# Kernel tuning notes

Hardware: AMD Instinct MI355X
Metric: run time of the kernel (lower is better)

## Reference

```python
import jax, jax.numpy as jnp
import numpy as np

NUM_NODES = 50000
NUM_EDGES = 600000
IN_DIM = 128
OUT_DIM = 128


def setup_inputs() -> dict:
    key = jax.random.key(0)
    k1, k2, k3, k4, k5 = jax.random.split(key, 5)
    x = jax.random.normal(k1, (NUM_NODES, IN_DIM), dtype=jnp.float32)
    edge_index = jax.random.randint(k2, (2, NUM_EDGES), 0, NUM_NODES, dtype=jnp.int64)
    edge_weight = jax.random.uniform(k3, (NUM_EDGES,), dtype=jnp.float32)
    W = jax.random.normal(k4, (OUT_DIM, IN_DIM), dtype=jnp.float32) * (1.0 / np.sqrt(IN_DIM))
    b = jax.random.normal(k5, (OUT_DIM,), dtype=jnp.float32) * 0.01
    return {"x": x, "edge_index": edge_index, "edge_weight": edge_weight, "W": W, "b": b}


def reference(x, edge_index, edge_weight, W, b):
    num_nodes = x.shape[0]
    # add self loops
    loop = jnp.arange(num_nodes, dtype=edge_index.dtype)
    src = jnp.concatenate([edge_index[0], loop])           # [E + N]
    tgt = jnp.concatenate([edge_index[1], loop])           # [E + N]
    w = jnp.concatenate([edge_weight, jnp.ones((num_nodes,), dtype=edge_weight.dtype)])
    # degree via scatter-add over src, then symmetric normalization
    deg = jax.ops.segment_sum(w, src, num_segments=num_nodes)  # [N]
    dinv = 1.0 / jnp.sqrt(deg)
    w_norm = w * dinv[src] * dinv[tgt]                      # [E + N]
    # gather-scale-scatter aggregation
    msg = x[src] * w_norm[:, None]                          # [E + N, D]
    agg = jax.ops.segment_sum(msg, tgt, num_segments=num_nodes)  # [N, D]
    # dense linear (torch Linear convention)
    return agg @ W.T + b
```

## Files before the change

### kernel.cpp

```cpp
#include <hip/hip_runtime.h>

#define D 128
#define GROWS 32
#define HCHUNKS 128
#define RNG 8064


__device__ __forceinline__ unsigned bf16rne(float f) {
  unsigned u = __float_as_uint(f);
  return (u + 0x7FFFu + ((u >> 16) & 1u)) >> 16;
}

__device__ __forceinline__ float4 bf16x4(uint2 u) {
  float4 r;
  r.x = __uint_as_float(u.x << 16);
  r.y = __uint_as_float(u.x & 0xFFFF0000u);
  r.z = __uint_as_float(u.y << 16);
  r.w = __uint_as_float(u.y & 0xFFFF0000u);
  return r;
}

__global__ __launch_bounds__(256) void k_setup(const float* __restrict__ W,
                                               const int* __restrict__ ei,
                                               float* __restrict__ Wt,
                                               int* __restrict__ flag) {
  int i = blockIdx.x * 256 + threadIdx.x;
  if (i < D * D) {
    int c = i >> 7, k = i & 127;
    Wt[k * D + c] = W[i];
  }
  if (i == 0) {
    flag[0] = (ei[1] == 0 && ei[3] == 0 && ei[5] == 0 && ei[7] == 0) ? 1 : 0;
  }
}

__global__ __launch_bounds__(256) void k_gemm(const float* __restrict__ x,
                                              const float* __restrict__ Wt,
                                              uint2* __restrict__ yb,
                                              int N) {
  __shared__ float Xs[GROWS * D];
  const int tid = threadIdx.x;
  const int row0 = blockIdx.x * GROWS;

  for (int f = tid; f < GROWS * D / 4; f += 256) {
    int r = row0 + ((f * 4) >> 7);
    float4 v = make_float4(0.f, 0.f, 0.f, 0.f);
    if (r < N)
      v = reinterpret_cast<const float4*>(x)[(size_t)row0 * (D / 4) + f];
    reinterpret_cast<float4*>(Xs)[f] = v;
  }
  __syncthreads();

  const int c0 = (tid & 31) * 4;
  const int r0 = (tid >> 5) * 4;
  float acc[4][4];
#pragma unroll
  for (int i = 0; i < 4; ++i)
#pragma unroll
    for (int j = 0; j < 4; ++j) acc[i][j] = 0.f;

#pragma unroll 4
  for (int k = 0; k < D; ++k) {
    float4 wv = reinterpret_cast<const float4*>(Wt)[(k * D + c0) >> 2];
    float xr[4];
#pragma unroll
    for (int i = 0; i < 4; ++i) xr[i] = Xs[(r0 + i) * D + k];
#pragma unroll
    for (int i = 0; i < 4; ++i) {
      acc[i][0] += xr[i] * wv.x;
      acc[i][1] += xr[i] * wv.y;
      acc[i][2] += xr[i] * wv.z;
      acc[i][3] += xr[i] * wv.w;
    }
  }
#pragma unroll
  for (int i = 0; i < 4; ++i) {
    int row = row0 + r0 + i;
    if (row < N) {
      uint2 u;
      u.x = bf16rne(acc[i][0]) | (bf16rne(acc[i][1]) << 16);
      u.y = bf16rne(acc[i][2]) | (bf16rne(acc[i][3]) << 16);
      yb[(size_t)row * 32 + (tid & 31)] = u;
    }
  }
}

__global__ __launch_bounds__(256) void k_hist(const int* __restrict__ ei,
                                              const float* __restrict__ ew,
                                              float* __restrict__ pdeg,
                                              unsigned short* __restrict__ pcnt,
                                              const int* __restrict__ flag,
                                              int E) {
  __shared__ float hd[RNG];
  __shared__ int hc[RNG];
  const int tid = threadIdx.x;
  const int chunk = blockIdx.x, r = blockIdx.y;
  const int lo = r * RNG;
  for (int i = tid; i < RNG; i += 256) { hd[i] = 0.f; hc[i] = 0; }
  __syncthreads();

  const int epc = (E + HCHUNKS - 1) / HCHUNKS;
  const int e0 = chunk * epc;
  const int e1 = min(e0 + epc, E);
  const bool f64 = flag[0] != 0;
  const int2* ei2 = reinterpret_cast<const int2*>(ei);
  for (int e = e0 + tid; e < e1; e += 256) {
    int s = f64 ? ei2[e].x : ei[e];
    int t = f64 ? ei2[E + e].x : ei[E + e];
    int ds = s - lo;
    if ((unsigned)ds < (unsigned)RNG) atomicAdd(&hd[ds], ew[e]);
    int dt = t - lo;
    if ((unsigned)dt < (unsigned)RNG) atomicAdd(&hc[dt], 1);
  }
  __syncthreads();
  size_t base = ((size_t)r * HCHUNKS + chunk) * RNG;
  for (int i = tid; i < RNG; i += 256) {
    pdeg[base + i] = hd[i];
    pcnt[base + i] = (unsigned short)hc[i];
  }
}

__device__ __forceinline__ int wave_incl_scan(int v, int lane) {
#pragma unroll
  for (int o = 1; o < 64; o <<= 1) {
    int t = __shfl_up(v, o);
    if (lane >= o) v += t;
  }
  return v;
}

__global__ __launch_bounds__(256) void k_scan1(const float* __restrict__ pdeg,
                                               const unsigned short* __restrict__ pcnt,
                                               float* __restrict__ dinv,
                                               int* __restrict__ rowptr,
                                               int* __restrict__ blocksum,
                                               int N) {
  __shared__ int wtot[4];
  int tid = threadIdx.x;
  int i = blockIdx.x * 256 + tid;
  int v = 0;
  if (i < N) {
    int r = i / RNG, off = i - r * RNG;
    size_t base = (size_t)r * HCHUNKS * RNG + off;
    float s = 0.f;
    int c = 0;
#pragma unroll 8
    for (int k = 0; k < HCHUNKS; ++k) {
      s += pdeg[base + (size_t)k * RNG];
      c += pcnt[base + (size_t)k * RNG];
    }
    dinv[i] = rsqrtf(s + 1.0f);
    v = c;
  }
  int lane = tid & 63, wv = tid >> 6;
  int inc = wave_incl_scan(v, lane);
  if (lane == 63) wtot[wv] = inc;
  __syncthreads();
  if (tid == 0) {
    int r = 0;
#pragma unroll
    for (int k = 0; k < 4; ++k) { int t = wtot[k]; wtot[k] = r; r += t; }
  }
  __syncthreads();
  int exc = wtot[wv] + inc - v;
  if (i < N) rowptr[i] = exc;
  if (tid == 255) blocksum[blockIdx.x] = wtot[3] + inc;
}

__global__ __launch_bounds__(64) void k_scan2(int* __restrict__ blocksum,
                                              int* __restrict__ blockoff,
                                              int nb) {
  int lane = threadIdx.x;
  int carry = 0;
  for (int base = 0; base < nb; base += 64) {
    int idx = base + lane;
    int v = (idx < nb) ? blocksum[idx] : 0;
    int inc = wave_incl_scan(v, lane);
    if (idx < nb) blockoff[idx] = carry + inc - v;
    carry += __shfl(inc, 63);
  }
}

__global__ __launch_bounds__(256) void k_scan3base(int* __restrict__ rowptr,
                                                   const int* __restrict__ blockoff,
                                                   const unsigned short* __restrict__ pcnt,
                                                   int* __restrict__ cbase,
                                                   int N, int E) {
  int i = blockIdx.x * 256 + threadIdx.x;
  if (i >= N) {
    if (i == N) rowptr[N] = E;
    return;
  }
  int rp = rowptr[i] + blockoff[blockIdx.x];
  rowptr[i] = rp;
  int r = i / RNG, off = i - r * RNG;
  size_t pb = (size_t)r * HCHUNKS * RNG + off;
  int run = rp;
#pragma unroll 8
  for (int c = 0; c < HCHUNKS; ++c) {
    cbase[(size_t)c * N + i] = run;
    run += pcnt[pb + (size_t)c * RNG];
  }
}

__global__ __launch_bounds__(256) void k_scatter(const int* __restrict__ ei,
                                                 const float* __restrict__ ew,
                                                 const float* __restrict__ dinv,
                                                 const int* __restrict__ cbase,
                                                 int2* __restrict__ edges,
                                                 const int* __restrict__ flag,
                                                 int N, int E) {
  __shared__ int hb[RNG];
  const int tid = threadIdx.x;
  const int chunk = blockIdx.x, r = blockIdx.y;
  const int lo = r * RNG;
  for (int j = tid; j < RNG; j += 256) {
    int v = lo + j;
    hb[j] = (v < N) ? cbase[(size_t)chunk * N + v] : 0;
  }
  __syncthreads();

  const int epc = (E + HCHUNKS - 1) / HCHUNKS;
  const int e0 = chunk * epc;
  const int e1 = min(e0 + epc, E);
  const bool f64 = flag[0] != 0;
  const int2* ei2 = reinterpret_cast<const int2*>(ei);
  for (int e = e0 + tid; e < e1; e += 256) {
    int t = f64 ? ei2[E + e].x : ei[E + e];
    int dt = t - lo;
    if ((unsigned)dt < (unsigned)RNG) {
      int s = f64 ? ei2[e].x : ei[e];
      int pos = atomicAdd(&hb[dt], 1);
      edges[pos] = make_int2(s, __float_as_int(ew[e] * dinv[s]));
    }
  }
}

__global__ __launch_bounds__(256) void k_gather(const int* __restrict__ rowptr,
                                                const int2* __restrict__ edges,
                                                const uint2* __restrict__ yb,
                                                const float* __restrict__ dinv,
                                                const float* __restrict__ b,
                                                float* __restrict__ out,
                                                int N) {
  const int tid = threadIdx.x;
  const int node = blockIdx.x * 4 + (tid >> 6);
  if (node >= N) return;
  const int lane = tid & 63, half = lane >> 5, l32 = lane & 31;

  const float dt = dinv[node];
  const float4 yself = bf16x4(yb[(size_t)node * 32 + l32]);
  const float4 bb = reinterpret_cast<const float4*>(b)[l32];

  float4 acc = make_float4(0.f, 0.f, 0.f, 0.f);
  const int end = rowptr[node + 1];
  int e = rowptr[node] + half;
  for (; e + 6 < end; e += 8) {
    int2 e0 = edges[e], e1 = edges[e + 2], e2 = edges[e + 4], e3 = edges[e + 6];
    float4 v0 = bf16x4(yb[(size_t)e0.x * 32 + l32]);
    float4 v1 = bf16x4(yb[(size_t)e1.x * 32 + l32]);
    float4 v2 = bf16x4(yb[(size_t)e2.x * 32 + l32]);
    float4 v3 = bf16x4(yb[(size_t)e3.x * 32 + l32]);
    float w0 = __int_as_float(e0.y), w1 = __int_as_float(e1.y);
    float w2 = __int_as_float(e2.y), w3 = __int_as_float(e3.y);
    acc.x += w0 * v0.x; acc.y += w0 * v0.y; acc.z += w0 * v0.z; acc.w += w0 * v0.w;
    acc.x += w1 * v1.x; acc.y += w1 * v1.y; acc.z += w1 * v1.z; acc.w += w1 * v1.w;
    acc.x += w2 * v2.x; acc.y += w2 * v2.y; acc.z += w2 * v2.z; acc.w += w2 * v2.w;
    acc.x += w3 * v3.x; acc.y += w3 * v3.y; acc.z += w3 * v3.z; acc.w += w3 * v3.w;
  }
  for (; e < end; e += 2) {
    int2 e0 = edges[e];
    float4 v0 = bf16x4(yb[(size_t)e0.x * 32 + l32]);
    float w0 = __int_as_float(e0.y);
    acc.x += w0 * v0.x; acc.y += w0 * v0.y; acc.z += w0 * v0.z; acc.w += w0 * v0.w;
  }
  acc.x += __shfl(acc.x, l32 + 32);
  acc.y += __shfl(acc.y, l32 + 32);
  acc.z += __shfl(acc.z, l32 + 32);
  acc.w += __shfl(acc.w, l32 + 32);
  if (half == 0) {
    float4 r;
    r.x = bb.x + dt * (acc.x + dt * yself.x);
    r.y = bb.y + dt * (acc.y + dt * yself.y);
    r.z = bb.z + dt * (acc.z + dt * yself.z);
    r.w = bb.w + dt * (acc.w + dt * yself.w);
    reinterpret_cast<float4*>(out)[(size_t)node * 32 + l32] = r;
  }
}

extern "C" void kernel_launch(void* const* d_in, const int* in_sizes, int n_in,
                              void* d_out, int out_size, void* d_ws, size_t ws_size,
                              hipStream_t stream) {
  const float* x = (const float*)d_in[0];
  const int* ei = (const int*)d_in[1];
  const float* ew = (const float*)d_in[2];
  const float* W = (const float*)d_in[3];
  const float* b = (const float*)d_in[4];
  float* out = (float*)d_out;

  const int N = in_sizes[0] / D;
  const int E = in_sizes[2];
  const int NB = (N + 255) / 256;
  const int nr = (N + RNG - 1) / RNG;

  char* ws = (char*)d_ws;
  size_t off = 0;
  auto alloc = [&](size_t bytes) {
    char* p = ws + off;
    off = (off + bytes + 255) & ~(size_t)255;
    return p;
  };
  float* Wt = (float*)alloc((size_t)D * D * 4);
  uint2* yb = (uint2*)alloc((size_t)N * D * 2);
  float* dinv = (float*)alloc((size_t)N * 4);
  float* pdeg = (float*)alloc((size_t)nr * HCHUNKS * RNG * 4);
  unsigned short* pcnt =
      (unsigned short*)alloc((size_t)nr * HCHUNKS * RNG * 2);
  int* cbase = (int*)alloc((size_t)HCHUNKS * N * 4);
  int* rowptr = (int*)alloc((size_t)(N + 1) * 4);
  int* blocksum = (int*)alloc((size_t)NB * 4);
  int* blockoff = (int*)alloc((size_t)NB * 4);
  int2* edges = (int2*)alloc((size_t)E * 8);
  int* flag = (int*)alloc(4);

  hipLaunchKernelGGL(k_setup, dim3((D * D + 255) / 256), dim3(256), 0, stream,
                     W, ei, Wt, flag);
  hipLaunchKernelGGL(k_gemm, dim3((N + GROWS - 1) / GROWS), dim3(256), 0,
                     stream, x, Wt, yb, N);
  hipLaunchKernelGGL(k_hist, dim3(HCHUNKS, nr), dim3(256), 0, stream,
                     ei, ew, pdeg, pcnt, flag, E);
  hipLaunchKernelGGL(k_scan1, dim3(NB), dim3(256), 0, stream,
                     pdeg, pcnt, dinv, rowptr, blocksum, N);
  hipLaunchKernelGGL(k_scan2, dim3(1), dim3(64), 0, stream,
                     blocksum, blockoff, NB);
  hipLaunchKernelGGL(k_scan3base, dim3(NB + 1), dim3(256), 0, stream,
                     rowptr, blockoff, pcnt, cbase, N, E);
  hipLaunchKernelGGL(k_scatter, dim3(HCHUNKS, nr), dim3(256), 0, stream,
                     ei, ew, dinv, cbase, edges, flag, N, E);
  hipLaunchKernelGGL(k_gather, dim3((N + 3) / 4), dim3(256), 0, stream,
                     rowptr, edges, yb, dinv, b, out, N);
}
```

Before: 223.0 us.

## Use bf16 MFMA for GEMM and fold block-offset scan into base kernel

Replaces the FP32 scalar GEMM with a bf16 MFMA 16x16x32 kernel, using a pre-packed bf16 weight layout and a bf16 shared tile for x. It also removes the single-block scan2 launch by having each scan3base block reduce the preceding block sums itself. The gather reads row pointers from the first cbase row instead of a separate rowptr pass. Quantizing x to bf16 before the matmul adds precision loss, and each scan block redundantly reads blocksums.

```diff
diff --git a/kernel.cpp b/kernel.cpp
--- a/kernel.cpp
+++ b/kernel.cpp
@@ -1,9 +1,11 @@
 #include <hip/hip_runtime.h>
 
 #define D 128
-#define GROWS 32
 #define HCHUNKS 128
 #define RNG 8064
+
+typedef __attribute__((ext_vector_type(8))) short bf16x8;
+typedef __attribute__((ext_vector_type(4))) float f32x4;
 
 
 __device__ __forceinline__ unsigned bf16rne(float f) {
@@ -11,7 +13,7 @@
   return (u + 0x7FFFu + ((u >> 16) & 1u)) >> 16;
 }
 
-__device__ __forceinline__ float4 bf16x4(uint2 u) {
+__device__ __forceinline__ float4 bf16x4u(uint2 u) {
   float4 r;
   r.x = __uint_as_float(u.x << 16);
   r.y = __uint_as_float(u.x & 0xFFFF0000u);
@@ -22,65 +24,79 @@
 
 __global__ __launch_bounds__(256) void k_setup(const float* __restrict__ W,
                                                const int* __restrict__ ei,
-                                               float* __restrict__ Wt,
+                                               unsigned short* __restrict__ Wtb,
                                                int* __restrict__ flag) {
-  int i = blockIdx.x * 256 + threadIdx.x;
-  if (i < D * D) {
-    int c = i >> 7, k = i & 127;
-    Wt[k * D + c] = W[i];
-  }
-  if (i == 0) {
+  int t = blockIdx.x * 256 + threadIdx.x;
+  int lane = t & 63;
+  int k0 = (t >> 6) & 3;
+  int n0 = t >> 8;
+  int n = n0 * 16 + (lane & 15);
+  int kb = k0 * 32 + ((lane >> 4) << 3);
+  const float4* wr = reinterpret_cast<const float4*>(W + n * D + kb);
+  float4 a = wr[0], c = wr[1];
+  unsigned short* dst = Wtb + (size_t)t * 8;
+  dst[0] = bf16rne(a.x); dst[1] = bf16rne(a.y);
+  dst[2] = bf16rne(a.z); dst[3] = bf16rne(a.w);
+  dst[4] = bf16rne(c.x); dst[5] = bf16rne(c.y);
+  dst[6] = bf16rne(c.z); dst[7] = bf16rne(c.w);
+  if (t == 0) {
     flag[0] = (ei[1] == 0 && ei[3] == 0 && ei[5] == 0 && ei[7] == 0) ? 1 : 0;
   }
 }
 
 __global__ __launch_bounds__(256) void k_gemm(const float* __restrict__ x,
-                                              const float* __restrict__ Wt,
-                                              uint2* __restrict__ yb,
+                                              const unsigned short* __restrict__ Wtb,
+                                              unsigned short* __restrict__ ybs,
                                               int N) {
-  __shared__ float Xs[GROWS * D];
-  const int tid = threadIdx.x;
-  const int row0 = blockIdx.x * GROWS;
-
-  for (int f = tid; f < GROWS * D / 4; f += 256) {
-    int r = row0 + ((f * 4) >> 7);
+  __shared__ unsigned short XA[4 * 4 * 64 * 8];
+  __shared__ unsigned short WB[8 * 4 * 64 * 8];
+  const int tid = threadIdx.x;
+  const int row0 = blockIdx.x * 64;
+
+  {
+    const uint4* src = reinterpret_cast<const uint4*>(Wtb);
+    uint4* dst = reinterpret_cast<uint4*>(WB);
+#pragma unroll
+    for (int k = 0; k < 8; ++k) dst[tid + k * 256] = src[tid + k * 256];
+  }
+  for (int idx = tid; idx < 64 * 32; idx += 256) {
+    int row = idx >> 5;
+    int c4 = (idx & 31) * 4;
     float4 v = make_float4(0.f, 0.f, 0.f, 0.f);
-    if (r < N)
-      v = reinterpret_cast<const float4*>(x)[(size_t)row0 * (D / 4) + f];
-    reinterpret_cast<float4*>(Xs)[f] = v;
-  }
-  __syncthreads();
-
-  const int c0 = (tid & 31) * 4;
-  const int r0 = (tid >> 5) * 4;
-  float acc[4][4];
-#pragma unroll
-  for (int i = 0; i < 4; ++i)
-#pragma unroll
-    for (int j = 0; j < 4; ++j) acc[i][j] = 0.f;
-
-#pragma unroll 4
-  for (int k = 0; k < D; ++k) {
-    float4 wv = reinterpret_cast<const float4*>(Wt)[(k * D + c0) >> 2];
-    float xr[4];
-#pragma unroll
-    for (int i = 0; i < 4; ++i) xr[i] = Xs[(r0 + i) * D + k];
-#pragma unroll
-    for (int i = 0; i < 4; ++i) {
-      acc[i][0] += xr[i] * wv.x;
-      acc[i][1] += xr[i] * wv.y;
-      acc[i][2] += xr[i] * wv.z;
-      acc[i][3] += xr[i] * wv.w;
+    int grow = row0 + row;
+    if (grow < N)
+      v = reinterpret_cast<const float4*>(x)[((size_t)grow * D + c4) >> 2];
+    int g = row >> 4, mr = row & 15;
+    int k0 = c4 >> 5, quad = (c4 >> 3) & 3, j = c4 & 7;
+    unsigned short* p =
+        &XA[(((g * 4 + k0) * 64) + quad * 16 + mr) * 8 + j];
+    p[0] = bf16rne(v.x); p[1] = bf16rne(v.y);
+    p[2] = bf16rne(v.z); p[3] = bf16rne(v.w);
+  }
+  __syncthreads();
+
+  const int g = tid >> 6, lane = tid & 63;
+  bf16x8 a[4];
+#pragma unroll
+  for (int k0 = 0; k0 < 4; ++k0)
+    a[k0] = *reinterpret_cast<const bf16x8*>(&XA[((g * 4 + k0) * 64 + lane) * 8]);
+
+  const int colb = lane & 15;
+  const int rbase = row0 + g * 16 + ((lane >> 4) << 2);
+#pragma unroll
+  for (int n0 = 0; n0 < 8; ++n0) {
+    f32x4 acc = {0.f, 0.f, 0.f, 0.f};
+#pragma unroll
+    for (int k0 = 0; k0 < 4; ++k0) {
+      bf16x8 bfr =
+          *reinterpret_cast<const bf16x8*>(&WB[((n0 * 4 + k0) * 64 + lane) * 8]);
+      acc = __builtin_amdgcn_mfma_f32_16x16x32_bf16(a[k0], bfr, acc, 0, 0, 0);
     }
-  }
-#pragma unroll
-  for (int i = 0; i < 4; ++i) {
-    int row = row0 + r0 + i;
-    if (row < N) {
-      uint2 u;
-      u.x = bf16rne(acc[i][0]) | (bf16rne(acc[i][1]) << 16);
-      u.y = bf16rne(acc[i][2]) | (bf16rne(acc[i][3]) << 16);
-      yb[(size_t)row * 32 + (tid & 31)] = u;
+    int col = n0 * 16 + colb;
+#pragma unroll
+    for (int reg = 0; reg < 4; ++reg) {
+      int row = rbase + reg;
+      if (row < N) ybs[(size_t)row * D + col] = (unsigned short)bf16rne(acc[reg]);
     }
   }
 }
@@ -167,35 +183,27 @@
   if (tid == 255) blocksum[blockIdx.x] = wtot[3] + inc;
 }
 
-__global__ __launch_bounds__(64) void k_scan2(int* __restrict__ blocksum,
-                                              int* __restrict__ blockoff,
-                                              int nb) {
-  int lane = threadIdx.x;
-  int carry = 0;
-  for (int base = 0; base < nb; base += 64) {
-    int idx = base + lane;
-    int v = (idx < nb) ? blocksum[idx] : 0;
-    int inc = wave_incl_scan(v, lane);
-    if (idx < nb) blockoff[idx] = carry + inc - v;
-    carry += __shfl(inc, 63);
-  }
-}
-
-__global__ __launch_bounds__(256) void k_scan3base(int* __restrict__ rowptr,
-                                                   const int* __restrict__ blockoff,
+__global__ __launch_bounds__(256) void k_scan3base(const int* __restrict__ rowptr,
+                                                   const int* __restrict__ blocksum,
                                                    const unsigned short* __restrict__ pcnt,
                                                    int* __restrict__ cbase,
-                                                   int N, int E) {
-  int i = blockIdx.x * 256 + threadIdx.x;
-  if (i >= N) {
-    if (i == N) rowptr[N] = E;
-    return;
-  }
-  int rp = rowptr[i] + blockoff[blockIdx.x];
-  rowptr[i] = rp;
+                                                   int N) {
+  __shared__ int sboff;
+  const int tid = threadIdx.x;
+  const int bid = blockIdx.x;
+  if (tid < 64) {
+    int s = 0;
+    for (int k = tid; k < bid; k += 64) s += blocksum[k];
+#pragma unroll
+    for (int o = 1; o < 64; o <<= 1) s += __shfl_xor(s, o);
+    if (tid == 0) sboff = s;
+  }
+  __syncthreads();
+  int i = bid * 256 + tid;
+  if (i >= N) return;
+  int run = rowptr[i] + sboff;
   int r = i / RNG, off = i - r * RNG;
   size_t pb = (size_t)r * HCHUNKS * RNG + off;
-  int run = rp;
 #pragma unroll 8
   for (int c = 0; c < HCHUNKS; ++c) {
     cbase[(size_t)c * N + i] = run;
@@ -236,31 +244,31 @@
   }
 }
 
-__global__ __launch_bounds__(256) void k_gather(const int* __restrict__ rowptr,
+__global__ __launch_bounds__(256) void k_gather(const int* __restrict__ rp0,
                                                 const int2* __restrict__ edges,
                                                 const uint2* __restrict__ yb,
                                                 const float* __restrict__ dinv,
                                                 const float* __restrict__ b,
                                                 float* __restrict__ out,
-                                                int N) {
+                                                int N, int E) {
   const int tid = threadIdx.x;
   const int node = blockIdx.x * 4 + (tid >> 6);
   if (node >= N) return;
   const int lane = tid & 63, half = lane >> 5, l32 = lane & 31;
 
   const float dt = dinv[node];
-  const float4 yself = bf16x4(yb[(size_t)node * 32 + l32]);
+  const float4 yself = bf16x4u(yb[(size_t)node * 32 + l32]);
   const float4 bb = reinterpret_cast<const float4*>(b)[l32];
 
   float4 acc = make_float4(0.f, 0.f, 0.f, 0.f);
-  const int end = rowptr[node + 1];
-  int e = rowptr[node] + half;
+  const int end = (node + 1 < N) ? rp0[node + 1] : E;
+  int e = rp0[node] + half;
   for (; e + 6 < end; e += 8) {
     int2 e0 = edges[e], e1 = edges[e + 2], e2 = edges[e + 4], e3 = edges[e + 6];
-    float4 v0 = bf16x4(yb[(size_t)e0.x * 32 + l32]);
-    float4 v1 = bf16x4(yb[(size_t)e1.x * 32 + l32]);
-    float4 v2 = bf16x4(yb[(size_t)e2.x * 32 + l32]);
-    float4 v3 = bf16x4(yb[(size_t)e3.x * 32 + l32]);
+    float4 v0 = bf16x4u(yb[(size_t)e0.x * 32 + l32]);
+    float4 v1 = bf16x4u(yb[(size_t)e1.x * 32 + l32]);
+    float4 v2 = bf16x4u(yb[(size_t)e2.x * 32 + l32]);
+    float4 v3 = bf16x4u(yb[(size_t)e3.x * 32 + l32]);
     float w0 = __int_as_float(e0.y), w1 = __int_as_float(e1.y);
     float w2 = __int_as_float(e2.y), w3 = __int_as_float(e3.y);
     acc.x += w0 * v0.x; acc.y += w0 * v0.y; acc.z += w0 * v0.z; acc.w += w0 * v0.w;
@@ -270,7 +278,7 @@
   }
   for (; e < end; e += 2) {
     int2 e0 = edges[e];
-    float4 v0 = bf16x4(yb[(size_t)e0.x * 32 + l32]);
+    float4 v0 = bf16x4u(yb[(size_t)e0.x * 32 + l32]);
     float w0 = __int_as_float(e0.y);
     acc.x += w0 * v0.x; acc.y += w0 * v0.y; acc.z += w0 * v0.z; acc.w += w0 * v0.w;
   }
@@ -310,33 +318,29 @@
     off = (off + bytes + 255) & ~(size_t)255;
     return p;
   };
-  float* Wt = (float*)alloc((size_t)D * D * 4);
+  unsigned short* Wtb = (unsigned short*)alloc((size_t)D * D * 2);
   uint2* yb = (uint2*)alloc((size_t)N * D * 2);
   float* dinv = (float*)alloc((size_t)N * 4);
   float* pdeg = (float*)alloc((size_t)nr * HCHUNKS * RNG * 4);
   unsigned short* pcnt =
       (unsigned short*)alloc((size_t)nr * HCHUNKS * RNG * 2);
   int* cbase = (int*)alloc((size_t)HCHUNKS * N * 4);
-  int* rowptr = (int*)alloc((size_t)(N + 1) * 4);
+  int* rowptr = (int*)alloc((size_t)N * 4);
   int* blocksum = (int*)alloc((size_t)NB * 4);
-  int* blockoff = (int*)alloc((size_t)NB * 4);
   int2* edges = (int2*)alloc((size_t)E * 8);
   int* flag = (int*)alloc(4);
 
-  hipLaunchKernelGGL(k_setup, dim3((D * D + 255) / 256), dim3(256), 0, stream,
-                     W, ei, Wt, flag);
-  hipLaunchKernelGGL(k_gemm, dim3((N + GROWS - 1) / GROWS), dim3(256), 0,
-                     stream, x, Wt, yb, N);
+  hipLaunchKernelGGL(k_setup, dim3(8), dim3(256), 0, stream, W, ei, Wtb, flag);
+  hipLaunchKernelGGL(k_gemm, dim3((N + 63) / 64), dim3(256), 0, stream,
+                     x, Wtb, (unsigned short*)yb, N);
   hipLaunchKernelGGL(k_hist, dim3(HCHUNKS, nr), dim3(256), 0, stream,
                      ei, ew, pdeg, pcnt, flag, E);
   hipLaunchKernelGGL(k_scan1, dim3(NB), dim3(256), 0, stream,
                      pdeg, pcnt, dinv, rowptr, blocksum, N);
-  hipLaunchKernelGGL(k_scan2, dim3(1), dim3(64), 0, stream,
-                     blocksum, blockoff, NB);
-  hipLaunchKernelGGL(k_scan3base, dim3(NB + 1), dim3(256), 0, stream,
-                     rowptr, blockoff, pcnt, cbase, N, E);
+  hipLaunchKernelGGL(k_scan3base, dim3(NB), dim3(256), 0, stream,
+                     rowptr, blocksum, pcnt, cbase, N);
   hipLaunchKernelGGL(k_scatter, dim3(HCHUNKS, nr), dim3(256), 0, stream,
                      ei, ew, dinv, cbase, edges, flag, N, E);
   hipLaunchKernelGGL(k_gather, dim3((N + 3) / 4), dim3(256), 0, stream,
-                     rowptr, edges, yb, dinv, b, out, N);
-}
+                     cbase, edges, yb, dinv, b, out, N, E);
+}
```

Measured after the change: 199.7 us. 1.12x faster.
